# Optimization experiments

Measured on AMD Instinct MI355X. Metric: run time of the kernel, lower is better.

Reference implementation:

```python
import jax, jax.numpy as jnp
import numpy as np

D = 512        # latent_dim
DT = 256       # text_latent_dim
H = 8          # num_heads
TE = 2048      # time_embed_dim
NEG = -1000000.0


def _ln(x, g, b, eps=1e-5):
    m = jnp.mean(x, axis=-1, keepdims=True)
    v = jnp.mean(jnp.square(x - m), axis=-1, keepdims=True)
    return (x - m) * jax.lax.rsqrt(v + eps) * g + b


def _linear(x, W, b):
    return x @ W.T + b


def setup_inputs() -> dict:
    key = jax.random.key(0)
    ks = jax.random.split(key, 24)
    B, T, NT, R, LR = 32, 1024, 77, 4, 256
    inp = {
        'x': jax.random.normal(ks[0], (B, T, D), jnp.float32),
        'xf': jax.random.normal(ks[1], (B, NT, DT), jnp.float32),
        'emb': jax.random.normal(ks[2], (B, TE), jnp.float32),
        'src_mask': jax.random.randint(ks[3], (B, T, 1), 0, 2).astype(jnp.float32),
        'cond_type': jax.random.randint(ks[4], (B, 1, 1), 0, 100).astype(jnp.int32),
        're_motion': jax.random.normal(ks[5], (B, R, LR, D), jnp.float32),
        're_text': jax.random.normal(ks[6], (B, R, 1, D), jnp.float32),
        're_mask': jax.random.randint(ks[7], (B, R, LR), 0, 2).astype(jnp.float32),
    }
    s = 0.02
    def W(k, o, i):
        return jax.random.normal(k, (o, i), jnp.float32) * s
    params = {
        'norm_g': jnp.ones((D,), jnp.float32), 'norm_b': jnp.zeros((D,), jnp.float32),
        'tnorm_g': jnp.ones((DT,), jnp.float32), 'tnorm_b': jnp.zeros((DT,), jnp.float32),
        'rn1_g': jnp.ones((2 * D,), jnp.float32), 'rn1_b': jnp.zeros((2 * D,), jnp.float32),
        'rn2_g': jnp.ones((D,), jnp.float32), 'rn2_b': jnp.zeros((D,), jnp.float32),
        'Wq': W(ks[8], D, D), 'bq': jnp.zeros((D,), jnp.float32),
        'Wkt': W(ks[9], D, DT), 'bkt': jnp.zeros((D,), jnp.float32),
        'Wvt': W(ks[10], D, DT), 'bvt': jnp.zeros((D,), jnp.float32),
        'Wkm': W(ks[11], D, D), 'bkm': jnp.zeros((D,), jnp.float32),
        'Wvm': W(ks[12], D, D), 'bvm': jnp.zeros((D,), jnp.float32),
        'Wkr': W(ks[13], D, 2 * D), 'bkr': jnp.zeros((D,), jnp.float32),
        'Wvr': W(ks[14], D, D), 'bvr': jnp.zeros((D,), jnp.float32),
        'emb_W': W(ks[15], 2 * D, TE), 'emb_b': jnp.zeros((2 * D,), jnp.float32),
        'snorm_g': jnp.ones((D,), jnp.float32), 'snorm_b': jnp.zeros((D,), jnp.float32),
        'out_W': W(ks[16], D, D), 'out_b': jnp.zeros((D,), jnp.float32),
    }
    inp.update(params)
    return inp


def _forward(x, xf, emb, src_mask, cond_type, re_motion, re_text, re_mask,
             norm_g, norm_b, tnorm_g, tnorm_b, rn1_g, rn1_b, rn2_g, rn2_b,
             Wq, bq, Wkt, bkt, Wvt, bvt, Wkm, bkm, Wvm, bvm, Wkr, bkr, Wvr, bvr,
             emb_W, emb_b, snorm_g, snorm_b, out_W, out_b):
    B, T, _ = x.shape
    re_mask_r = re_mask.reshape(B, -1, 1)                       # [B, R*LR, 1]
    N = xf.shape[1] + T + re_motion.shape[1] * re_motion.shape[2]

    xn = _ln(x, norm_g, norm_b)                                  # [B,T,D]
    xfn = _ln(xf, tnorm_g, tnorm_b)                              # [B,NT,DT]
    query = _linear(xn, Wq, bq)                                  # [B,T,D]

    text_ct = (cond_type % 10 > 0).astype(x.dtype)               # [B,1,1]
    retr_ct = (cond_type // 10 > 0).astype(x.dtype)              # [B,1,1]

    re_text_rep = jnp.broadcast_to(re_text, re_motion.shape)     # repeat along Lr
    re_feat_key = jnp.concatenate([re_motion, re_text_rep], axis=-1).reshape(B, -1, 2 * D)

    k_text = _linear(xfn, Wkt, bkt) + (1.0 - text_ct) * NEG
    k_retr = (_linear(_ln(re_feat_key, rn1_g, rn1_b), Wkr, bkr)
              + (1.0 - retr_ct) * NEG + (1.0 - re_mask_r) * NEG)
    k_mot = _linear(xn, Wkm, bkm) + (1.0 - src_mask) * NEG
    key_cat = jnp.concatenate([k_text, k_retr, k_mot], axis=1)   # [B,N,D]

    q = jax.nn.softmax(query.reshape(B, T, H, -1), axis=-1)      # softmax over head_dim
    k = jax.nn.softmax(key_cat.reshape(B, N, H, -1), axis=1)     # softmax over tokens

    re_feat_value = re_motion.reshape(B, -1, D)
    v_text = _linear(xfn, Wvt, bvt) * text_ct
    v_retr = _linear(_ln(re_feat_value, rn2_g, rn2_b), Wvr, bvr) * retr_ct * re_mask_r
    v_mot = _linear(xn, Wvm, bvm) * src_mask
    v = jnp.concatenate([v_text, v_retr, v_mot], axis=1).reshape(B, N, H, -1)

    attention = jnp.einsum('bnhd,bnhl->bhdl', k, v)              # [B,H,hd,hd]
    y = jnp.einsum('bthd,bhdl->bthl', q, attention).reshape(B, T, D)

    # StylizationBlock: film-style scale/shift from time embedding, zero-init out proj
    emb_out = _linear(jax.nn.silu(emb), emb_W, emb_b)[:, None, :]  # [B,1,2D]
    scale, shift = emb_out[..., :D], emb_out[..., D:]
    h = _ln(y, snorm_g, snorm_b) * (1.0 + scale) + shift
    h = _linear(jax.nn.silu(h), out_W, out_b)
    return x + h


def reference(x, xf, emb, src_mask, cond_type, re_motion, re_text, re_mask,
              norm_g, norm_b, tnorm_g, tnorm_b, rn1_g, rn1_b, rn2_g, rn2_b,
              Wq, bq, Wkt, bkt, Wvt, bvt, Wkm, bkm, Wvm, bvm, Wkr, bkr, Wvr, bvr,
              emb_W, emb_b, snorm_g, snorm_b, out_W, out_b):
    return _forward(x, xf, emb, src_mask, cond_type, re_motion, re_text, re_mask,
                    norm_g, norm_b, tnorm_g, tnorm_b, rn1_g, rn1_b, rn2_g, rn2_b,
                    Wq, bq, Wkt, bkt, Wvt, bvt, Wkm, bkm, Wvm, bvm, Wkr, bkr, Wvr, bvr,
                    emb_W, emb_b, snorm_g, snorm_b, out_W, out_b)
```

## Files before the change

### kernel.cpp

```cpp
#include <hip/hip_runtime.h>
#include <cstddef>
#include <cstdint>

#define DEV __device__ __forceinline__

namespace {

constexpr int kH = 8;
constexpr int kB = 32, kT = 1024, kNT = 77, kR = 4, kLR = 256;
constexpr int kRL = kR * kLR;
constexpr float kNEG = -1000000.0f;
constexpr int kNtot = 2304;
constexpr int kNS2 = 3;
constexpr int kLDSW = 136;

typedef __bf16 bf16x8 __attribute__((ext_vector_type(8)));
typedef float f32x4 __attribute__((ext_vector_type(4)));

DEV unsigned short f2bf(float f) {
  unsigned int u = __float_as_uint(f);
  u += 0x7fffu + ((u >> 16) & 1u);
  return (unsigned short)(u >> 16);
}
DEV float bf2f(unsigned short h) { return __uint_as_float(((unsigned int)h) << 16); }

DEV float wave_sum(float v) {
  #pragma unroll
  for (int s = 32; s; s >>= 1) v += __shfl_xor(v, s);
  return v;
}

template<int COLS>
__global__ __launch_bounds__(256) void ln_bf16(const float* __restrict__ in,
    const float* __restrict__ g, const float* __restrict__ be,
    unsigned short* __restrict__ out) {
  constexpr int PT = COLS / 256;
  int row = blockIdx.x;
  const float* p = in + (size_t)row * COLS;
  unsigned short* o = out + (size_t)row * COLS;
  float v[PT]; float s = 0.f, s2 = 0.f;
  #pragma unroll
  for (int i = 0; i < PT; i++) {
    v[i] = p[threadIdx.x + i * 256];
    s += v[i]; s2 += v[i] * v[i];
  }
  __shared__ float red[2][4];
  int lane = threadIdx.x & 63, w = threadIdx.x >> 6;
  s = wave_sum(s); s2 = wave_sum(s2);
  if (!lane) { red[0][w] = s; red[1][w] = s2; }
  __syncthreads();
  s = red[0][0] + red[0][1] + red[0][2] + red[0][3];
  s2 = red[1][0] + red[1][1] + red[1][2] + red[1][3];
  float mean = s / COLS;
  float var = s2 / COLS - mean * mean;
  float rstd = rsqrtf(var + 1e-5f);
  #pragma unroll
  for (int i = 0; i < PT; i++) {
    int c = threadIdx.x + i * 256;
    o[c] = f2bf((v[i] - mean) * rstd * g[c] + be[c]);
  }
}

__global__ __launch_bounds__(256) void rfk_norm(const float* __restrict__ mot,
    const float* __restrict__ txt,
    const float* __restrict__ g1, const float* __restrict__ b1,
    const float* __restrict__ g2, const float* __restrict__ b2,
    unsigned short* __restrict__ rfk, unsigned short* __restrict__ rfv) {
  int m = blockIdx.x;
  const float* pm = mot + (size_t)m * 512;
  const float* pt = txt + (size_t)(m >> 8) * 512;
  float v[2], t[2];
  float sv = 0.f, sv2 = 0.f, st = 0.f, st2 = 0.f;
  #pragma unroll
  for (int i = 0; i < 2; i++) {
    v[i] = pm[threadIdx.x + i * 256]; sv += v[i]; sv2 += v[i] * v[i];
    t[i] = pt[threadIdx.x + i * 256]; st += t[i]; st2 += t[i] * t[i];
  }
  __shared__ float red[4][4];
  int lane = threadIdx.x & 63, w = threadIdx.x >> 6;
  sv = wave_sum(sv); sv2 = wave_sum(sv2); st = wave_sum(st); st2 = wave_sum(st2);
  if (!lane) { red[0][w] = sv; red[1][w] = sv2; red[2][w] = st; red[3][w] = st2; }
  __syncthreads();
  float SV = red[0][0] + red[0][1] + red[0][2] + red[0][3];
  float SV2 = red[1][0] + red[1][1] + red[1][2] + red[1][3];
  float ST = red[2][0] + red[2][1] + red[2][2] + red[2][3];
  float ST2 = red[3][0] + red[3][1] + red[3][2] + red[3][3];
  float SA = SV + ST, SA2 = SV2 + ST2;
  float ma = SA / 1024.f, va = SA2 / 1024.f - ma * ma;
  float ra_ = rsqrtf(va + 1e-5f);
  float mv = SV / 512.f, vv = SV2 / 512.f - mv * mv;
  float rv_ = rsqrtf(vv + 1e-5f);
  #pragma unroll
  for (int i = 0; i < 2; i++) {
    int c = threadIdx.x + i * 256;
    rfk[(size_t)m * 1024 + c]       = f2bf((v[i] - ma) * ra_ * g1[c] + b1[c]);
    rfk[(size_t)m * 1024 + 512 + c] = f2bf((t[i] - ma) * ra_ * g1[512 + c] + b1[512 + c]);
    rfv[(size_t)m * 512 + c]        = f2bf((v[i] - mv) * rv_ * g2[c] + b2[c]);
  }
}

__global__ __launch_bounds__(256) void rowmask_kernel(const int* __restrict__ ct,
    const float* __restrict__ src_mask, const float* __restrict__ re_mask,
    float* __restrict__ kaT, float* __restrict__ kaR, float* __restrict__ kaM,
    float* __restrict__ vmT, float* __restrict__ vmR, float* __restrict__ vmM,
    int nB) {
  int i = blockIdx.x * 256 + threadIdx.x;
  if (i < nB * kRL) {
    int b = i >> 10;
    int c = ct[b];
    float retr = (c / 10 > 0) ? 1.f : 0.f;
    float rm = re_mask[i];
    kaR[i] = (1.f - retr) * kNEG + (1.f - rm) * kNEG;
    vmR[i] = retr * rm;
    float sm = src_mask[i];
    kaM[i] = (1.f - sm) * kNEG;
    vmM[i] = sm;
  }
  if (i < nB * kNT) {
    int b = i / kNT;
    int c = ct[b];
    float text = (c % 10 > 0) ? 1.f : 0.f;
    kaT[i] = (1.f - text) * kNEG;
    vmT[i] = text;
  }
}

__global__ __launch_bounds__(256) void castw(const float* __restrict__ s,
    unsigned short* __restrict__ d, int n) {
  int i = (blockIdx.x * 256 + threadIdx.x) * 4;
  if (i < n) {
    float4 v = *reinterpret_cast<const float4*>(s + i);
    ushort4 o;
    o.x = f2bf(v.x); o.y = f2bf(v.y); o.z = f2bf(v.z); o.w = f2bf(v.w);
    *reinterpret_cast<ushort4*>(d + i) = o;
  }
}

__global__ __launch_bounds__(256) void zpad_kernel(unsigned short* __restrict__ E,
    unsigned short* __restrict__ V, int rows) {
  int i = blockIdx.x * 256 + threadIdx.x;
  if (i >= rows * 24) return;
  int row = i / 24, c = i % 24;
  size_t off = (size_t)row * kNtot + 2112 + c * 8;
  ulonglong2 z; z.x = 0; z.y = 0;
  *reinterpret_cast<ulonglong2*>(E + off) = z;
  *reinterpret_cast<ulonglong2*>(V + off) = z;
}

__global__ __launch_bounds__(256) void silu_emb(const float* __restrict__ emb,
    float* __restrict__ semb) {
  int i = (blockIdx.x * 256 + threadIdx.x) * 4;
  float4 v = *reinterpret_cast<const float4*>(emb + i);
  float4 o;
  o.x = v.x / (1.f + __expf(-v.x));
  o.y = v.y / (1.f + __expf(-v.y));
  o.z = v.z / (1.f + __expf(-v.z));
  o.w = v.w / (1.f + __expf(-v.w));
  *reinterpret_cast<float4*>(semb + i) = o;
}

__global__ __launch_bounds__(256) void emb_gemv2(const float* __restrict__ semb,
    const float* __restrict__ W, float* __restrict__ part) {
  int n = blockIdx.x * 4 + (threadIdx.x >> 6);
  int s = blockIdx.y;
  int lane = threadIdx.x & 63;
  int k = s * 256 + lane * 4;
  float4 wv = *reinterpret_cast<const float4*>(&W[(size_t)n * 2048 + k]);
  float acc[32];
  #pragma unroll
  for (int m = 0; m < 32; m++) {
    float4 sv = *reinterpret_cast<const float4*>(&semb[(size_t)m * 2048 + k]);
    acc[m] = fmaf(sv.x, wv.x, fmaf(sv.y, wv.y, fmaf(sv.z, wv.z, sv.w * wv.w)));
  }
  #pragma unroll
  for (int m = 0; m < 32; m++) {
    float t = wave_sum(acc[m]);
    if (lane == 0) part[((size_t)s * 32 + m) * 1024 + n] = t;
  }
}
__global__ __launch_bounds__(256) void emb_fin(const float* __restrict__ part,
    const float* __restrict__ bias, float* __restrict__ ss) {
  int i = blockIdx.x * 256 + threadIdx.x;
  float s = 0.f;
  #pragma unroll
  for (int c = 0; c < 8; c++) s += part[(size_t)c * 32768 + i];
  ss[i] = s + bias[i & 1023];
}

template<int OUTMODE, int TR>
__global__ __launch_bounds__(256) void gemm_mfma(
    const unsigned short* __restrict__ A, const unsigned short* __restrict__ W,
    const float* __restrict__ bias, void* __restrict__ Cout,
    int M, int K, int m_per_b, int n_total, int out_off,
    const float* __restrict__ rowAdd, const float* __restrict__ rowMul,
    const float* __restrict__ addX) {
  __shared__ __align__(16) char smem[34816];
  unsigned short* lds = (unsigned short*)smem;
  const int tid = threadIdx.x;
  const int lane = tid & 63;
  const int wv = tid >> 6;
  const int wr = (wv >> 1) * 64;
  const int wc = (wv & 1) * 64;
  const int m0 = blockIdx.y * 128;
  const int n0 = blockIdx.x * 128;

  const unsigned short* srcA[2]; const unsigned short* srcB[2];
  int dstOff[2];
  #pragma unroll
  for (int i = 0; i < 2; i++) {
    int lin = i * 256 + tid;
    int r = lin >> 2, cl = lin & 3;
    int cs = cl ^ ((r >> 1) & 3);
    int ra = m0 + r; if (ra > M - 1) ra = M - 1;
    srcA[i] = A + (size_t)ra * K + cs * 8;
    srcB[i] = W + (size_t)(n0 + r) * K + cs * 8;
    dstOff[i] = lin * 8;
  }
  int offA[4], offB[4];
  #pragma unroll
  for (int i = 0; i < 4; i++) {
    int r = wr + i * 16 + (lane & 15);
    int c = (lane >> 4) ^ ((r >> 1) & 3);
    offA[i] = r * 32 + c * 8;
    int rb = wc + i * 16 + (lane & 15);
    int cb = (lane >> 4) ^ ((rb >> 1) & 3);
    offB[i] = rb * 32 + cb * 8;
  }

  f32x4 acc[4][4] = {};

  #pragma unroll
  for (int i = 0; i < 2; i++) {
    __builtin_amdgcn_global_load_lds(
        (const __attribute__((address_space(1))) void*)(srcA[i]),
        (__attribute__((address_space(3))) void*)&lds[dstOff[i]], 16, 0, 0);
    __builtin_amdgcn_global_load_lds(
        (const __attribute__((address_space(1))) void*)(srcB[i]),
        (__attribute__((address_space(3))) void*)&lds[4096 + dstOff[i]], 16, 0, 0);
  }
  __syncthreads();

  int c = 0;
  for (int k0 = 0; k0 < K; k0 += 32) {
    int nc = c ^ 1;
    if (k0 + 32 < K) {
      #pragma unroll
      for (int i = 0; i < 2; i++) {
        __builtin_amdgcn_global_load_lds(
            (const __attribute__((address_space(1))) void*)(srcA[i] + k0 + 32),
            (__attribute__((address_space(3))) void*)&lds[nc * 8192 + dstOff[i]], 16, 0, 0);
        __builtin_amdgcn_global_load_lds(
            (const __attribute__((address_space(1))) void*)(srcB[i] + k0 + 32),
            (__attribute__((address_space(3))) void*)&lds[nc * 8192 + 4096 + dstOff[i]], 16, 0, 0);
      }
    }
    bf16x8 af[4], bf[4];
    #pragma unroll
    for (int i = 0; i < 4; i++) {
      af[i] = *reinterpret_cast<const bf16x8*>(&lds[c * 8192 + offA[i]]);
      bf[i] = *reinterpret_cast<const bf16x8*>(&lds[c * 8192 + 4096 + offB[i]]);
    }
    #pragma unroll
    for (int i = 0; i < 4; i++)
      #pragma unroll
      for (int j = 0; j < 4; j++)
        acc[i][j] = __builtin_amdgcn_mfma_f32_16x16x32_bf16(af[i], bf[j], acc[i][j], 0, 0, 0);
    __syncthreads();
    c = nc;
  }

  const int r4 = (lane >> 4) << 2;
  const int colb = n0 + wc + (lane & 15);
  const int rowb = m0 + wr + r4;

  if (OUTMODE != 0 && TR && (m_per_b & 7)) {
    unsigned short* C16 = (unsigned short*)Cout;
    #pragma unroll
    for (int i = 0; i < 4; i++) {
      #pragma unroll
      for (int r = 0; r < 4; r++) {
        int row = rowb + i * 16 + r;
        if (row >= M) continue;
        float ra = rowAdd ? rowAdd[row] : 0.f;
        float rm = rowMul ? rowMul[row] : 1.f;
        size_t nn = out_off + (row % m_per_b);
        size_t cb = (size_t)(row / m_per_b) * 512;
        #pragma unroll
        for (int j = 0; j < 4; j++) {
          int col = colb + j * 16;
          float v = (acc[i][j][r] + bias[col] + ra) * rm;
          if (OUTMODE == 2) v = __expf(v);
          C16[(cb + col) * kNtot + nn] = f2bf(v);
        }
      }
    }
    return;
  }

  if (OUTMODE != 0) {
    unsigned short* S = (unsigned short*)smem;
    #pragma unroll
    for (int i = 0; i < 4; i++) {
      #pragma unroll
      for (int r = 0; r < 4; r++) {
        int row_t = wr + i * 16 + r4 + r;
        int rowg = m0 + row_t; if (rowg > M - 1) rowg = M - 1;
        float ra = rowAdd ? rowAdd[rowg] : 0.f;
        float rm = rowMul ? rowMul[rowg] : 1.f;
        int key = TR ? (((row_t >> 3) & 7) << 3) : 0;
        #pragma unroll
        for (int j = 0; j < 4; j++) {
          int col_t = wc + j * 16 + (lane & 15);
          float v = (acc[i][j][r] + bias[n0 + col_t] + ra) * rm;
          if (OUTMODE == 2) v = __expf(v);
          S[row_t * kLDSW + (col_t ^ key)] = f2bf(v);
        }
      }
    }
    __syncthreads();
    if (TR) {
      #pragma unroll
      for (int it = 0; it < 8; it++) {
        int slot = it * 256 + tid;
        int col_t = slot >> 4;
        int mcx = slot & 15;
        int mc = mcx * 8;
        int key = (mcx & 7) << 3;
        union { unsigned short u[8]; ulonglong2 v; } w;
        #pragma unroll
        for (int e = 0; e < 8; e++)
          w.u[e] = S[(mc + e) * kLDSW + (col_t ^ key)];
        int row = m0 + mc;
        size_t obase = ((size_t)(row / m_per_b) * 512 + n0 + col_t) * (size_t)kNtot
                     + out_off + (row % m_per_b);
        *reinterpret_cast<ulonglong2*>((unsigned short*)Cout + obase) = w.v;
      }
    } else {
      #pragma unroll
      for (int it = 0; it < 8; it++) {
        int slot = it * 256 + tid;
        int row_t = slot >> 4;
        int cs = (slot & 15) * 8;
        int row = m0 + row_t;
        if (row < M) {
          size_t orow = (size_t)(row / m_per_b) * n_total + out_off + (row % m_per_b);
          ulonglong2 d = *reinterpret_cast<const ulonglong2*>(&S[row_t * kLDSW + cs]);
          *reinterpret_cast<ulonglong2*>((unsigned short*)Cout + orow * 512 + n0 + cs) = d;
        }
      }
    }
  } else {
    float* Sf = (float*)smem;
    #pragma unroll
    for (int p = 0; p < 2; p++) {
      __syncthreads();
      #pragma unroll
      for (int i2 = 0; i2 < 2; i2++) {
        int i = p * 2 + i2;
        #pragma unroll
        for (int r = 0; r < 4; r++) {
          int row_t = wr + i * 16 + r4 + r;
          int srow = (row_t & 31) + ((row_t >> 6) << 5);
          int rowg = m0 + row_t; if (rowg > M - 1) rowg = M - 1;
          float ra = rowAdd ? rowAdd[rowg] : 0.f;
          float rm = rowMul ? rowMul[rowg] : 1.f;
          #pragma unroll
          for (int j = 0; j < 4; j++) {
            int col_t = wc + j * 16 + (lane & 15);
            Sf[srow * kLDSW + col_t] = (acc[i][j][r] + bias[n0 + col_t] + ra) * rm;
          }
        }
      }
      __syncthreads();
      #pragma unroll
      for (int it = 0; it < 8; it++) {
        int slot = it * 256 + tid;
        int srow = slot >> 5;
        int c4 = (slot & 31) * 4;
        int row_t = (srow & 31) + p * 32 + ((srow >> 5) << 6);
        int row = m0 + row_t;
        if (row < M) {
          size_t orow = (size_t)(row / m_per_b) * n_total + out_off + (row % m_per_b);
          float4 v = *reinterpret_cast<const float4*>(&Sf[srow * kLDSW + c4]);
          if (addX) {
            float4 xv = *reinterpret_cast<const float4*>(&addX[(size_t)row * 512 + n0 + c4]);
            v.x += xv.x; v.y += xv.y; v.z += xv.z; v.w += xv.w;
          }
          *reinterpret_cast<float4*>((float*)Cout + orow * 512 + n0 + c4) = v;
        }
      }
    }
  }
}

__global__ __launch_bounds__(256) void attp_kernel(const unsigned short* __restrict__ E,
    const unsigned short* __restrict__ V, float* __restrict__ part,
    float* __restrict__ part_cs) {
  int bh = blockIdx.x;
  int s = blockIdx.y;
  const unsigned short* Ep = E + (size_t)bh * 64 * kNtot;
  const unsigned short* Vp = V + (size_t)bh * 64 * kNtot;
  __shared__ __align__(16) char smem[34816];
  unsigned short* Elds = (unsigned short*)smem;
  unsigned short* Vlds = (unsigned short*)(smem + 17408);
  int tid = threadIdx.x, lane = tid & 63, wv = tid >> 6;
  f32x4 acc[4] = {};
  float csum = 0.f;
  int cd = tid & 63, cq = tid >> 6;
  const int arow = (wv * 16 + (lane & 15)) * 136 + ((lane >> 4) << 3);
  const int brow0 = ((lane & 15)) * 136 + ((lane >> 4) << 3);

  for (int it = 0; it < 6; it++) {
    int n0 = s * 768 + it * 128;
    __syncthreads();
    #pragma unroll
    for (int r = 0; r < 4; r++) {
      int ch = r * 256 + tid;
      int d = ch >> 4, off = (ch & 15) * 8;
      *reinterpret_cast<ulonglong2*>(&Elds[d * 136 + off]) =
          *reinterpret_cast<const ulonglong2*>(Ep + (size_t)d * kNtot + n0 + off);
      *reinterpret_cast<ulonglong2*>(&Vlds[d * 136 + off]) =
          *reinterpret_cast<const ulonglong2*>(Vp + (size_t)d * kNtot + n0 + off);
    }
    __syncthreads();
    #pragma unroll
    for (int ks = 0; ks < 4; ks++) {
      bf16x8 af = *reinterpret_cast<const bf16x8*>(&Elds[arow + ks * 32]);
      #pragma unroll
      for (int j = 0; j < 4; j++) {
        bf16x8 bf = *reinterpret_cast<const bf16x8*>(&Vlds[brow0 + j * 16 * 136 + ks * 32]);
        acc[j] = __builtin_amdgcn_mfma_f32_16x16x32_bf16(af, bf, acc[j], 0, 0, 0);
      }
    }
    #pragma unroll
    for (int k8 = 0; k8 < 4; k8++) {
      bf16x8 ev = *reinterpret_cast<const bf16x8*>(&Elds[cd * 136 + cq * 32 + k8 * 8]);
      const unsigned short* pu = reinterpret_cast<const unsigned short*>(&ev);
      #pragma unroll
      for (int e = 0; e < 8; e++) csum += bf2f(pu[e]);
    }
  }
  float* op = part + ((size_t)bh * kNS2 + s) * 4096;
  int dbase = wv * 16 + ((lane >> 4) << 2);
  #pragma unroll
  for (int j = 0; j < 4; j++)
    #pragma unroll
    for (int r = 0; r < 4; r++)
      op[(dbase + r) * 64 + j * 16 + (lane & 15)] = acc[j][r];
  __syncthreads();
  float* csu = (float*)smem;
  csu[cq * 64 + cd] = csum;
  __syncthreads();
  if (tid < 64)
    part_cs[((size_t)bh * kNS2 + s) * 64 + tid] =
        csu[tid] + csu[64 + tid] + csu[128 + tid] + csu[192 + tid];
}

__global__ __launch_bounds__(256) void attc_kernel(const float* __restrict__ part,
    const float* __restrict__ part_cs, unsigned short* __restrict__ attT) {
  int bh = blockIdx.x;
  __shared__ float at[64][65];
  __shared__ float sinv[64];
  int tid = threadIdx.x;
  if (tid < 64) {
    float s = 0.f;
    #pragma unroll
    for (int c = 0; c < kNS2; c++) s += part_cs[((size_t)bh * kNS2 + c) * 64 + tid];
    sinv[tid] = 1.f / s;
  }
  for (int i = tid; i < 4096; i += 256) {
    float s = 0.f;
    #pragma unroll
    for (int c = 0; c < kNS2; c++) s += part[((size_t)bh * kNS2 + c) * 4096 + i];
    at[i >> 6][i & 63] = s;
  }
  __syncthreads();
  for (int j = tid; j < 4096; j += 256) {
    int l = j >> 6, d = j & 63;
    attT[(size_t)bh * 4096 + j] = f2bf(at[d][l] * sinv[d]);
  }
}

__global__ __launch_bounds__(256) void y_mfma(const unsigned short* __restrict__ q,
    const unsigned short* __restrict__ attT, unsigned short* __restrict__ y) {
  int bh = blockIdx.x; int b = bh >> 3, h = bh & 7;
  int t0 = blockIdx.y * 128;
  __shared__ unsigned short bt[64][72];
  __shared__ float rs[128];
  __shared__ unsigned short ob[128][72];
  int tid = threadIdx.x, lane = tid & 63, wv = tid >> 6;
  int wr = wv * 32;
  for (int i = tid; i < 512; i += 256) {
    int row = i >> 3, c8 = (i & 7) * 8;
    *reinterpret_cast<ulonglong2*>(&bt[row][c8]) =
        *reinterpret_cast<const ulonglong2*>(attT + (size_t)bh * 4096 + row * 64 + c8);
  }
  const unsigned short* qp = q + ((size_t)(b * 1024 + t0 + wr)) * 512 + h * 64;
  bf16x8 af[2][2];
  #pragma unroll
  for (int i = 0; i < 2; i++) {
    int row = i * 16 + (lane & 15);
    #pragma unroll
    for (int s = 0; s < 2; s++)
      af[i][s] = *reinterpret_cast<const bf16x8*>(qp + (size_t)row * 512 + s * 32 + (lane >> 4) * 8);
  }
  #pragma unroll
  for (int i = 0; i < 2; i++) {
    float r = 0.f;
    #pragma unroll
    for (int s = 0; s < 2; s++) {
      const unsigned short* pu = reinterpret_cast<const unsigned short*>(&af[i][s]);
      #pragma unroll
      for (int e = 0; e < 8; e++) r += bf2f(pu[e]);
    }
    r += __shfl_xor(r, 16); r += __shfl_xor(r, 32);
    if (lane < 16) rs[wr + i * 16 + lane] = r;
  }
  __syncthreads();
  f32x4 acc[2][4] = {};
  #pragma unroll
  for (int s = 0; s < 2; s++) {
    #pragma unroll
    for (int j = 0; j < 4; j++) {
      bf16x8 bf = *reinterpret_cast<const bf16x8*>(&bt[j * 16 + (lane & 15)][s * 32 + (lane >> 4) * 8]);
      #pragma unroll
      for (int i = 0; i < 2; i++)
        acc[i][j] = __builtin_amdgcn_mfma_f32_16x16x32_bf16(af[i][s], bf, acc[i][j], 0, 0, 0);
    }
  }
  int r4 = (lane >> 4) << 2;
  #pragma unroll
  for (int i = 0; i < 2; i++) {
    #pragma unroll
    for (int r = 0; r < 4; r++) {
      int row = wr + i * 16 + r4 + r;
      float rinv = 1.f / rs[row];
      #pragma unroll
      for (int j = 0; j < 4; j++)
        ob[row][j * 16 + (lane & 15)] = f2bf(acc[i][j][r] * rinv);
    }
  }
  __syncthreads();
  for (int i = tid; i < 1024; i += 256) {
    int row = i >> 3, c8 = (i & 7) * 8;
    *reinterpret_cast<ulonglong2*>(y + ((size_t)(b * 1024 + t0 + row)) * 512 + h * 64 + c8) =
        *reinterpret_cast<const ulonglong2*>(&ob[row][c8]);
  }
}

__global__ __launch_bounds__(256) void mod_kernel(const unsigned short* __restrict__ y,
    const float* __restrict__ ss, const float* __restrict__ g, const float* __restrict__ be,
    unsigned short* __restrict__ h) {
  int row = blockIdx.x; int b = row >> 10;
  const unsigned short* p = y + (size_t)row * 512;
  unsigned short* o = h + (size_t)row * 512;
  float v[2]; float s = 0.f, s2 = 0.f;
  #pragma unroll
  for (int i = 0; i < 2; i++) {
    v[i] = bf2f(p[threadIdx.x + i * 256]);
    s += v[i]; s2 += v[i] * v[i];
  }
  __shared__ float red[2][4];
  int lane = threadIdx.x & 63, w = threadIdx.x >> 6;
  s = wave_sum(s); s2 = wave_sum(s2);
  if (!lane) { red[0][w] = s; red[1][w] = s2; }
  __syncthreads();
  s = red[0][0] + red[0][1] + red[0][2] + red[0][3];
  s2 = red[1][0] + red[1][1] + red[1][2] + red[1][3];
  float mean = s / 512.f, var = s2 / 512.f - mean * mean;
  float rstd = rsqrtf(var + 1e-5f);
  #pragma unroll
  for (int i = 0; i < 2; i++) {
    int c = threadIdx.x + i * 256;
    float val = (v[i] - mean) * rstd * g[c] + be[c];
    val = val * (1.f + ss[b * 1024 + c]) + ss[b * 1024 + 512 + c];
    o[c] = f2bf(val / (1.f + __expf(-val)));
  }
}

}

extern "C" void kernel_launch(void* const* d_in, const int* in_sizes, int n_in,
                              void* d_out, int out_size, void* d_ws, size_t ws_size,
                              hipStream_t stream) {
  const float* x        = (const float*)d_in[0];
  const float* xf       = (const float*)d_in[1];
  const float* emb      = (const float*)d_in[2];
  const float* src_mask = (const float*)d_in[3];
  const int*   cond     = (const int*)d_in[4];
  const float* re_motion= (const float*)d_in[5];
  const float* re_text  = (const float*)d_in[6];
  const float* re_mask  = (const float*)d_in[7];
  const float* norm_g = (const float*)d_in[8],  * norm_b = (const float*)d_in[9];
  const float* tnorm_g= (const float*)d_in[10], * tnorm_b= (const float*)d_in[11];
  const float* rn1_g  = (const float*)d_in[12], * rn1_b  = (const float*)d_in[13];
  const float* rn2_g  = (const float*)d_in[14], * rn2_b  = (const float*)d_in[15];
  const float* Wq  = (const float*)d_in[16], * bq  = (const float*)d_in[17];
  const float* Wkt = (const float*)d_in[18], * bkt = (const float*)d_in[19];
  const float* Wvt = (const float*)d_in[20], * bvt = (const float*)d_in[21];
  const float* Wkm = (const float*)d_in[22], * bkm = (const float*)d_in[23];
  const float* Wvm = (const float*)d_in[24], * bvm = (const float*)d_in[25];
  const float* Wkr = (const float*)d_in[26], * bkr = (const float*)d_in[27];
  const float* Wvr = (const float*)d_in[28], * bvr = (const float*)d_in[29];
  const float* emb_W = (const float*)d_in[30], * emb_b = (const float*)d_in[31];
  const float* snorm_g = (const float*)d_in[32], * snorm_b = (const float*)d_in[33];
  const float* out_W = (const float*)d_in[34], * out_b = (const float*)d_in[35];
  float* out = (float*)d_out;

  char* base = (char*)d_ws;
  size_t off = 0;
  auto ab = [&](size_t nb) { char* p = base + off; off = (off + nb + 255) & ~(size_t)255; return p; };

  unsigned short* wq_bf  = (unsigned short*)ab(512 * 512 * 2);
  unsigned short* wkt_bf = (unsigned short*)ab(512 * 256 * 2);
  unsigned short* wvt_bf = (unsigned short*)ab(512 * 256 * 2);
  unsigned short* wkm_bf = (unsigned short*)ab(512 * 512 * 2);
  unsigned short* wvm_bf = (unsigned short*)ab(512 * 512 * 2);
  unsigned short* wkr_bf = (unsigned short*)ab(512 * 1024 * 2);
  unsigned short* wvr_bf = (unsigned short*)ab(512 * 512 * 2);
  unsigned short* wout_bf= (unsigned short*)ab(512 * 512 * 2);
  float* semb_f   = (float*)ab((size_t)kB * 2048 * 4);
  float* part_emb = (float*)ab((size_t)8 * kB * 1024 * 4);
  float* ssb_full = (float*)ab((size_t)kB * 1024 * 4);
  float* kaT_full = (float*)ab((size_t)kB * kNT * 4);
  float* vmT_full = (float*)ab((size_t)kB * kNT * 4);
  float* kaR_full = (float*)ab((size_t)kB * kRL * 4);
  float* kaM_full = (float*)ab((size_t)kB * kT * 4);
  float* vmR_full = (float*)ab((size_t)kB * kRL * 4);
  float* vmM_full = (float*)ab((size_t)kB * kT * 4);
  const size_t fixed_off = off;

  auto pad = [](size_t n) { return (n + 255) & ~(size_t)255; };
  auto chunk_bytes = [&](size_t CH) -> size_t {
    size_t s = 0;
    s += pad(CH * 1024 * 512 * 2);
    s += pad(CH * kNT * 256 * 2);
    s += pad(CH * 1024 * 1024 * 2);
    s += pad(CH * 1024 * 512 * 2);
    s += pad(CH * 1024 * 512 * 2);
    s += pad((size_t)CH * 512 * kNtot * 2);
    s += pad((size_t)CH * 512 * kNtot * 2);
    s += pad(CH * 8 * 4096 * 2);
    s += pad(CH * 8 * (size_t)kNS2 * 4096 * 4);
    s += pad(CH * 8 * (size_t)kNS2 * 64 * 4);
    return s;
  };
  int CH = 32;
  while (CH > 1 && fixed_off + chunk_bytes(CH) > ws_size) CH >>= 1;

  auto cl = [&](const float* s, unsigned short* d, int n) {
    castw<<<dim3((n / 4 + 255) / 256), 256, 0, stream>>>(s, d, n);
  };
  cl(Wq,  wq_bf,  512 * 512);
  cl(Wkt, wkt_bf, 512 * 256);
  cl(Wvt, wvt_bf, 512 * 256);
  cl(Wkm, wkm_bf, 512 * 512);
  cl(Wvm, wvm_bf, 512 * 512);
  cl(Wkr, wkr_bf, 512 * 1024);
  cl(Wvr, wvr_bf, 512 * 512);
  cl(out_W, wout_bf, 512 * 512);

  rowmask_kernel<<<dim3(kB * 4), 256, 0, stream>>>(cond, src_mask, re_mask,
      kaT_full, kaR_full, kaM_full, vmT_full, vmR_full, vmM_full, kB);
  silu_emb<<<dim3(kB * 2048 / 1024), 256, 0, stream>>>(emb, semb_f);
  emb_gemv2<<<dim3(256, 8), 256, 0, stream>>>(semb_f, emb_W, part_emb);
  emb_fin<<<dim3(128), 256, 0, stream>>>(part_emb, emb_b, ssb_full);

  for (int b0 = 0; b0 < kB; b0 += CH) {
    off = fixed_off;
    const int MRc = CH * 1024;
    const int MTc = CH * kNT;

    unsigned short* xn_bf  = (unsigned short*)ab((size_t)MRc * 512 * 2);
    unsigned short* xfn_bf = (unsigned short*)ab((size_t)MTc * 256 * 2);
    unsigned short* rfk_bf = (unsigned short*)ab((size_t)MRc * 1024 * 2);
    unsigned short* rfv_bf = (unsigned short*)ab((size_t)MRc * 512 * 2);
    unsigned short* qb_bf  = (unsigned short*)ab((size_t)MRc * 512 * 2);
    unsigned short* kc_bf  = (unsigned short*)ab((size_t)CH * 512 * kNtot * 2);
    unsigned short* vb_bf  = (unsigned short*)ab((size_t)CH * 512 * kNtot * 2);
    unsigned short* attT = (unsigned short*)ab((size_t)CH * 8 * 4096 * 2);
    float* attp = (float*)ab((size_t)CH * 8 * kNS2 * 4096 * 4);
    float* part_cs = (float*)ab((size_t)CH * 8 * kNS2 * 64 * 4);
    unsigned short* yb16 = rfk_bf;
    unsigned short* h_bf = xn_bf;

    const float* x_c   = x + (size_t)b0 * kT * 512;
    const float* xf_c  = xf + (size_t)b0 * kNT * 256;
    const float* rm_c  = re_motion + (size_t)b0 * kRL * 512;
    const float* rt_c  = re_text + (size_t)b0 * kR * 512;
    float* out_c = out + (size_t)b0 * kT * 512;

    ln_bf16<512><<<dim3(MRc), 256, 0, stream>>>(x_c, norm_g, norm_b, xn_bf);
    ln_bf16<256><<<dim3(MTc), 256, 0, stream>>>(xf_c, tnorm_g, tnorm_b, xfn_bf);
    rfk_norm<<<dim3(MRc), 256, 0, stream>>>(rm_c, rt_c, rn1_g, rn1_b, rn2_g, rn2_b,
                                            rfk_bf, rfv_bf);
    zpad_kernel<<<dim3(CH * 48), 256, 0, stream>>>(kc_bf, vb_bf, CH * 512);

    gemm_mfma<2, 0><<<dim3(4, CH * 8), 256, 0, stream>>>(xn_bf, wq_bf, bq, qb_bf,
        MRc, 512, MRc, 0, 0, nullptr, nullptr, nullptr);
    gemm_mfma<2, 1><<<dim3(4, (MTc + 127) / 128), 256, 0, stream>>>(xfn_bf, wkt_bf, bkt, kc_bf,
        MTc, 256, kNT, 0, 0, kaT_full + (size_t)b0 * kNT, nullptr, nullptr);
    gemm_mfma<2, 1><<<dim3(4, CH * 8), 256, 0, stream>>>(rfk_bf, wkr_bf, bkr, kc_bf,
        MRc, 1024, kRL, 0, kNT, kaR_full + (size_t)b0 * kRL, nullptr, nullptr);
    gemm_mfma<2, 1><<<dim3(4, CH * 8), 256, 0, stream>>>(xn_bf, wkm_bf, bkm, kc_bf,
        MRc, 512, kT, 0, kNT + kRL, kaM_full + (size_t)b0 * kT, nullptr, nullptr);
    gemm_mfma<1, 1><<<dim3(4, (MTc + 127) / 128), 256, 0, stream>>>(xfn_bf, wvt_bf, bvt, vb_bf,
        MTc, 256, kNT, 0, 0, nullptr, vmT_full + (size_t)b0 * kNT, nullptr);
    gemm_mfma<1, 1><<<dim3(4, CH * 8), 256, 0, stream>>>(rfv_bf, wvr_bf, bvr, vb_bf,
        MRc, 512, kRL, 0, kNT, nullptr, vmR_full + (size_t)b0 * kRL, nullptr);
    gemm_mfma<1, 1><<<dim3(4, CH * 8), 256, 0, stream>>>(xn_bf, wvm_bf, bvm, vb_bf,
        MRc, 512, kT, 0, kNT + kRL, nullptr, vmM_full + (size_t)b0 * kT, nullptr);

    attp_kernel<<<dim3(CH * 8, kNS2), 256, 0, stream>>>(kc_bf, vb_bf, attp, part_cs);
    attc_kernel<<<dim3(CH * 8), 256, 0, stream>>>(attp, part_cs, attT);
    y_mfma<<<dim3(CH * 8, 8), 256, 0, stream>>>(qb_bf, attT, yb16);

    mod_kernel<<<dim3(MRc), 256, 0, stream>>>(yb16, ssb_full + (size_t)b0 * 1024,
                                              snorm_g, snorm_b, h_bf);
    gemm_mfma<0, 0><<<dim3(4, CH * 8), 256, 0, stream>>>(h_bf, wout_bf, out_b, out_c,
        MRc, 512, MRc, 0, 0, nullptr, nullptr, x_c);
  }
}
```

Before: 624.3 us.

## Fold retrieval LayerNorms into weights and apply row stats in GEMM epilogue

After: 648.8 us. +3.9%, slower.

```diff
diff --git a/kernel.cpp b/kernel.cpp
--- a/kernel.cpp
+++ b/kernel.cpp
@@ -61,11 +61,10 @@
   }
 }
 
-__global__ __launch_bounds__(256) void rfk_norm(const float* __restrict__ mot,
-    const float* __restrict__ txt,
-    const float* __restrict__ g1, const float* __restrict__ b1,
-    const float* __restrict__ g2, const float* __restrict__ b2,
-    unsigned short* __restrict__ rfk, unsigned short* __restrict__ rfv) {
+__global__ __launch_bounds__(256) void rfk_stats(const float* __restrict__ mot,
+    const float* __restrict__ txt, unsigned short* __restrict__ mot_bf,
+    float* __restrict__ s1k, float* __restrict__ s2k,
+    float* __restrict__ s1v, float* __restrict__ s2v) {
   int m = blockIdx.x;
   const float* pm = mot + (size_t)m * 512;
   const float* pt = txt + (size_t)(m >> 8) * 512;
@@ -81,21 +80,83 @@
   sv = wave_sum(sv); sv2 = wave_sum(sv2); st = wave_sum(st); st2 = wave_sum(st2);
   if (!lane) { red[0][w] = sv; red[1][w] = sv2; red[2][w] = st; red[3][w] = st2; }
   __syncthreads();
-  float SV = red[0][0] + red[0][1] + red[0][2] + red[0][3];
-  float SV2 = red[1][0] + red[1][1] + red[1][2] + red[1][3];
-  float ST = red[2][0] + red[2][1] + red[2][2] + red[2][3];
-  float ST2 = red[3][0] + red[3][1] + red[3][2] + red[3][3];
-  float SA = SV + ST, SA2 = SV2 + ST2;
-  float ma = SA / 1024.f, va = SA2 / 1024.f - ma * ma;
-  float ra_ = rsqrtf(va + 1e-5f);
-  float mv = SV / 512.f, vv = SV2 / 512.f - mv * mv;
-  float rv_ = rsqrtf(vv + 1e-5f);
-  #pragma unroll
-  for (int i = 0; i < 2; i++) {
-    int c = threadIdx.x + i * 256;
-    rfk[(size_t)m * 1024 + c]       = f2bf((v[i] - ma) * ra_ * g1[c] + b1[c]);
-    rfk[(size_t)m * 1024 + 512 + c] = f2bf((t[i] - ma) * ra_ * g1[512 + c] + b1[512 + c]);
-    rfv[(size_t)m * 512 + c]        = f2bf((v[i] - mv) * rv_ * g2[c] + b2[c]);
+  #pragma unroll
+  for (int i = 0; i < 2; i++)
+    mot_bf[(size_t)m * 512 + threadIdx.x + i * 256] = f2bf(v[i]);
+  if (threadIdx.x == 0) {
+    float SV = red[0][0] + red[0][1] + red[0][2] + red[0][3];
+    float SV2 = red[1][0] + red[1][1] + red[1][2] + red[1][3];
+    float ST = red[2][0] + red[2][1] + red[2][2] + red[2][3];
+    float ST2 = red[3][0] + red[3][1] + red[3][2] + red[3][3];
+    float SA = SV + ST, SA2 = SV2 + ST2;
+    float ma = SA / 1024.f, va = SA2 / 1024.f - ma * ma;
+    float ra = rsqrtf(va + 1e-5f);
+    float mv = SV / 512.f, vv = SV2 / 512.f - mv * mv;
+    float rv = rsqrtf(vv + 1e-5f);
+    s1k[m] = ra; s2k[m] = -ra * ma;
+    s1v[m] = rv; s2v[m] = -rv * mv;
+  }
+}
+
+__global__ __launch_bounds__(256) void prep_w(
+    const float* __restrict__ Wkr, const float* __restrict__ g1,
+    const float* __restrict__ b1, const float* __restrict__ bkr,
+    const float* __restrict__ Wvr, const float* __restrict__ g2,
+    const float* __restrict__ b2, const float* __restrict__ bvr,
+    unsigned short* __restrict__ w1lo, unsigned short* __restrict__ w2,
+    float* __restrict__ G1, float* __restrict__ B1,
+    float* __restrict__ G2, float* __restrict__ B2) {
+  int n = blockIdx.x;
+  int tid = threadIdx.x;
+  float gs = 0.f, bs = 0.f;
+  #pragma unroll
+  for (int i = 0; i < 4; i++) {
+    int k = tid + i * 256;
+    float w = Wkr[(size_t)n * 1024 + k];
+    float gv = g1[k];
+    gs += gv * w; bs += b1[k] * w;
+    if (i < 2) w1lo[(size_t)n * 512 + k] = f2bf(gv * w);
+  }
+  float g2s = 0.f, b2s = 0.f;
+  #pragma unroll
+  for (int i = 0; i < 2; i++) {
+    int k = tid + i * 256;
+    float w = Wvr[(size_t)n * 512 + k];
+    g2s += g2[k] * w; b2s += b2[k] * w;
+    w2[(size_t)n * 512 + k] = f2bf(g2[k] * w);
+  }
+  __shared__ float red[4][4];
+  int lane = tid & 63, w_ = tid >> 6;
+  gs = wave_sum(gs); bs = wave_sum(bs); g2s = wave_sum(g2s); b2s = wave_sum(b2s);
+  if (!lane) { red[0][w_] = gs; red[1][w_] = bs; red[2][w_] = g2s; red[3][w_] = b2s; }
+  __syncthreads();
+  if (tid == 0) {
+    G1[n] = red[0][0] + red[0][1] + red[0][2] + red[0][3];
+    B1[n] = red[1][0] + red[1][1] + red[1][2] + red[1][3] + bkr[n];
+    G2[n] = red[2][0] + red[2][1] + red[2][2] + red[2][3];
+    B2[n] = red[3][0] + red[3][1] + red[3][2] + red[3][3] + bvr[n];
+  }
+}
+
+__global__ __launch_bounds__(256) void text_T(const float* __restrict__ re_text,
+    const float* __restrict__ g1, const float* __restrict__ Wkr,
+    float* __restrict__ T) {
+  int m = blockIdx.x;
+  __shared__ float tr[512];
+  int tid = threadIdx.x;
+  #pragma unroll
+  for (int i = 0; i < 2; i++) {
+    int k = tid + i * 256;
+    tr[k] = re_text[(size_t)m * 512 + k] * g1[512 + k];
+  }
+  __syncthreads();
+  #pragma unroll
+  for (int i = 0; i < 2; i++) {
+    int n = tid + i * 256;
+    const float* wp = Wkr + (size_t)n * 1024 + 512;
+    float acc = 0.f;
+    for (int k = 0; k < 512; k++) acc = fmaf(tr[k], wp[k], acc);
+    T[(size_t)m * 512 + n] = acc;
   }
 }
 
@@ -187,13 +248,15 @@
   ss[i] = s + bias[i & 1023];
 }
 
-template<int OUTMODE, int TR>
+template<int OUTMODE, int TR, int EPI>
 __global__ __launch_bounds__(256) void gemm_mfma(
     const unsigned short* __restrict__ A, const unsigned short* __restrict__ W,
     const float* __restrict__ bias, void* __restrict__ Cout,
     int M, int K, int m_per_b, int n_total, int out_off,
     const float* __restrict__ rowAdd, const float* __restrict__ rowMul,
-    const float* __restrict__ addX) {
+    const float* __restrict__ addX,
+    const float* __restrict__ s1, const float* __restrict__ s2,
+    const float* __restrict__ Gv, const float* __restrict__ Tt) {
   __shared__ __align__(16) char smem[34816];
   unsigned short* lds = (unsigned short*)smem;
   const int tid = threadIdx.x;
@@ -273,6 +336,22 @@
   const int colb = n0 + wc + (lane & 15);
   const int rowb = m0 + wr + r4;
 
+  auto epival = [&](float accv, int rowg, int col) -> float {
+    float v;
+    if (EPI == 1) {
+      v = (accv + Tt[(size_t)(rowg >> 8) * 512 + col]) * s1[rowg]
+          + s2[rowg] * Gv[col] + bias[col] + rowAdd[rowg];
+    } else if (EPI == 2) {
+      v = (accv * s1[rowg] + s2[rowg] * Gv[col] + bias[col]) * rowMul[rowg];
+    } else {
+      float ra = rowAdd ? rowAdd[rowg] : 0.f;
+      float rm = rowMul ? rowMul[rowg] : 1.f;
+      v = (accv + bias[col] + ra) * rm;
+    }
+    if (OUTMODE == 2) v = __expf(v);
+    return v;
+  };
+
   if (OUTMODE != 0 && TR && (m_per_b & 7)) {
     unsigned short* C16 = (unsigned short*)Cout;
     #pragma unroll
@@ -281,16 +360,12 @@
       for (int r = 0; r < 4; r++) {
         int row = rowb + i * 16 + r;
         if (row >= M) continue;
-        float ra = rowAdd ? rowAdd[row] : 0.f;
-        float rm = rowMul ? rowMul[row] : 1.f;
         size_t nn = out_off + (row % m_per_b);
         size_t cb = (size_t)(row / m_per_b) * 512;
         #pragma unroll
         for (int j = 0; j < 4; j++) {
           int col = colb + j * 16;
-          float v = (acc[i][j][r] + bias[col] + ra) * rm;
-          if (OUTMODE == 2) v = __expf(v);
-          C16[(cb + col) * kNtot + nn] = f2bf(v);
+          C16[(cb + col) * kNtot + nn] = f2bf(epival(acc[i][j][r], row, col));
         }
       }
     }
@@ -305,15 +380,11 @@
       for (int r = 0; r < 4; r++) {
         int row_t = wr + i * 16 + r4 + r;
         int rowg = m0 + row_t; if (rowg > M - 1) rowg = M - 1;
-        float ra = rowAdd ? rowAdd[rowg] : 0.f;
-        float rm = rowMul ? rowMul[rowg] : 1.f;
         int key = TR ? (((row_t >> 3) & 7) << 3) : 0;
         #pragma unroll
         for (int j = 0; j < 4; j++) {
           int col_t = wc + j * 16 + (lane & 15);
-          float v = (acc[i][j][r] + bias[n0 + col_t] + ra) * rm;
-          if (OUTMODE == 2) v = __expf(v);
-          S[row_t * kLDSW + (col_t ^ key)] = f2bf(v);
+          S[row_t * kLDSW + (col_t ^ key)] = f2bf(epival(acc[i][j][r], rowg, n0 + col_t));
         }
       }
     }
@@ -362,11 +433,11 @@
           int row_t = wr + i * 16 + r4 + r;
           int srow = (row_t & 31) + ((row_t >> 6) << 5);
           int rowg = m0 + row_t; if (rowg > M - 1) rowg = M - 1;
-          float ra = rowAdd ? rowAdd[rowg] : 0.f;
-          float rm = rowMul ? rowMul[rowg] : 1.f;
           #pragma unroll
           for (int j = 0; j < 4; j++) {
             int col_t = wc + j * 16 + (lane & 15);
+            float ra = rowAdd ? rowAdd[rowg] : 0.f;
+            float rm = rowMul ? rowMul[rowg] : 1.f;
             Sf[srow * kLDSW + col_t] = (acc[i][j][r] + bias[n0 + col_t] + ra) * rm;
           }
         }
@@ -616,9 +687,12 @@
   unsigned short* wvt_bf = (unsigned short*)ab(512 * 256 * 2);
   unsigned short* wkm_bf = (unsigned short*)ab(512 * 512 * 2);
   unsigned short* wvm_bf = (unsigned short*)ab(512 * 512 * 2);
-  unsigned short* wkr_bf = (unsigned short*)ab(512 * 1024 * 2);
-  unsigned short* wvr_bf = (unsigned short*)ab(512 * 512 * 2);
   unsigned short* wout_bf= (unsigned short*)ab(512 * 512 * 2);
+  unsigned short* w1lo_bf= (unsigned short*)ab(512 * 512 * 2);
+  unsigned short* w2_bf  = (unsigned short*)ab(512 * 512 * 2);
+  float* G1 = (float*)ab(512 * 4); float* B1 = (float*)ab(512 * 4);
+  float* G2 = (float*)ab(512 * 4); float* B2 = (float*)ab(512 * 4);
+  float* Tbuf = (float*)ab((size_t)kB * kR * 512 * 4);
   float* semb_f   = (float*)ab((size_t)kB * 2048 * 4);
   float* part_emb = (float*)ab((size_t)8 * kB * 1024 * 4);
   float* ssb_full = (float*)ab((size_t)kB * 1024 * 4);
@@ -635,8 +709,8 @@
     size_t s = 0;
     s += pad(CH * 1024 * 512 * 2);
     s += pad(CH * kNT * 256 * 2);
-    s += pad(CH * 1024 * 1024 * 2);
     s += pad(CH * 1024 * 512 * 2);
+    s += 4 * pad(CH * 1024 * 4);
     s += pad(CH * 1024 * 512 * 2);
     s += pad((size_t)CH * 512 * kNtot * 2);
     s += pad((size_t)CH * 512 * kNtot * 2);
@@ -656,9 +730,10 @@
   cl(Wvt, wvt_bf, 512 * 256);
   cl(Wkm, wkm_bf, 512 * 512);
   cl(Wvm, wvm_bf, 512 * 512);
-  cl(Wkr, wkr_bf, 512 * 1024);
-  cl(Wvr, wvr_bf, 512 * 512);
   cl(out_W, wout_bf, 512 * 512);
+  prep_w<<<dim3(512), 256, 0, stream>>>(Wkr, rn1_g, rn1_b, bkr, Wvr, rn2_g, rn2_b, bvr,
+                                        w1lo_bf, w2_bf, G1, B1, G2, B2);
+  text_T<<<dim3(kB * kR), 256, 0, stream>>>(re_text, rn1_g, Wkr, Tbuf);
 
   rowmask_kernel<<<dim3(kB * 4), 256, 0, stream>>>(cond, src_mask, re_mask,
       kaT_full, kaR_full, kaM_full, vmT_full, vmR_full, vmM_full, kB);
@@ -673,15 +748,18 @@
 
     unsigned short* xn_bf  = (unsigned short*)ab((size_t)MRc * 512 * 2);
     unsigned short* xfn_bf = (unsigned short*)ab((size_t)MTc * 256 * 2);
-    unsigned short* rfk_bf = (unsigned short*)ab((size_t)MRc * 1024 * 2);
-    unsigned short* rfv_bf = (unsigned short*)ab((size_t)MRc * 512 * 2);
+    unsigned short* mot_bf = (unsigned short*)ab((size_t)MRc * 512 * 2);
+    float* s1k = (float*)ab((size_t)CH * 1024 * 4);
+    float* s2k = (float*)ab((size_t)CH * 1024 * 4);
+    float* s1v = (float*)ab((size_t)CH * 1024 * 4);
+    float* s2v = (float*)ab((size_t)CH * 1024 * 4);
     unsigned short* qb_bf  = (unsigned short*)ab((size_t)MRc * 512 * 2);
     unsigned short* kc_bf  = (unsigned short*)ab((size_t)CH * 512 * kNtot * 2);
     unsigned short* vb_bf  = (unsigned short*)ab((size_t)CH * 512 * kNtot * 2);
     unsigned short* attT = (unsigned short*)ab((size_t)CH * 8 * 4096 * 2);
     float* attp = (float*)ab((size_t)CH * 8 * kNS2 * 4096 * 4);
     float* part_cs = (float*)ab((size_t)CH * 8 * kNS2 * 64 * 4);
-    unsigned short* yb16 = rfk_bf;
+    unsigned short* yb16 = mot_bf;
     unsigned short* h_bf = xn_bf;
 
     const float* x_c   = x + (size_t)b0 * kT * 512;
@@ -692,24 +770,29 @@
 
     ln_bf16<512><<<dim3(MRc), 256, 0, stream>>>(x_c, norm_g, norm_b, xn_bf);
     ln_bf16<256><<<dim3(MTc), 256, 0, stream>>>(xf_c, tnorm_g, tnorm_b, xfn_bf);
-    rfk_norm<<<dim3(MRc), 256, 0, stream>>>(rm_c, rt_c, rn1_g, rn1_b, rn2_g, rn2_b,
-                                            rfk_bf, rfv_bf);
+    rfk_stats<<<dim3(MRc), 256, 0, stream>>>(rm_c, rt_c, mot_bf, s1k, s2k, s1v, s2v);
     zpad_kernel<<<dim3(CH * 48), 256, 0, stream>>>(kc_bf, vb_bf, CH * 512);
 
-    gemm_mfma<2, 0><<<dim3(4, CH * 8), 256, 0, stream>>>(xn_bf, wq_bf, bq, qb_bf,
-        MRc, 512, MRc, 0, 0, nullptr, nullptr, nullptr);
-    gemm_mfma<2, 1><<<dim3(4, (MTc + 127) / 128), 256, 0, stream>>>(xfn_bf, wkt_bf, bkt, kc_bf,
-        MTc, 256, kNT, 0, 0, kaT_full + (size_t)b0 * kNT, nullptr, nullptr);
-    gemm_mfma<2, 1><<<dim3(4, CH * 8), 256, 0, stream>>>(rfk_bf, wkr_bf, bkr, kc_bf,
-        MRc, 1024, kRL, 0, kNT, kaR_full + (size_t)b0 * kRL, nullptr, nullptr);
-    gemm_mfma<2, 1><<<dim3(4, CH * 8), 256, 0, stream>>>(xn_bf, wkm_bf, bkm, kc_bf,
-        MRc, 512, kT, 0, kNT + kRL, kaM_full + (size_t)b0 * kT, nullptr, nullptr);
-    gemm_mfma<1, 1><<<dim3(4, (MTc + 127) / 128), 256, 0, stream>>>(xfn_bf, wvt_bf, bvt, vb_bf,
-        MTc, 256, kNT, 0, 0, nullptr, vmT_full + (size_t)b0 * kNT, nullptr);
-    gemm_mfma<1, 1><<<dim3(4, CH * 8), 256, 0, stream>>>(rfv_bf, wvr_bf, bvr, vb_bf,
-        MRc, 512, kRL, 0, kNT, nullptr, vmR_full + (size_t)b0 * kRL, nullptr);
-    gemm_mfma<1, 1><<<dim3(4, CH * 8), 256, 0, stream>>>(xn_bf, wvm_bf, bvm, vb_bf,
-        MRc, 512, kT, 0, kNT + kRL, nullptr, vmM_full + (size_t)b0 * kT, nullptr);
+    gemm_mfma<2, 0, 0><<<dim3(4, CH * 8), 256, 0, stream>>>(xn_bf, wq_bf, bq, qb_bf,
+        MRc, 512, MRc, 0, 0, nullptr, nullptr, nullptr, nullptr, nullptr, nullptr, nullptr);
+    gemm_mfma<2, 1, 0><<<dim3(4, (MTc + 127) / 128), 256, 0, stream>>>(xfn_bf, wkt_bf, bkt, kc_bf,
+        MTc, 256, kNT, 0, 0, kaT_full + (size_t)b0 * kNT, nullptr, nullptr,
+        nullptr, nullptr, nullptr, nullptr);
+    gemm_mfma<2, 1, 1><<<dim3(4, CH * 8), 256, 0, stream>>>(mot_bf, w1lo_bf, B1, kc_bf,
+        MRc, 512, kRL, 0, kNT, kaR_full + (size_t)b0 * kRL, nullptr, nullptr,
+        s1k, s2k, G1, Tbuf + (size_t)b0 * kR * 512);
+    gemm_mfma<2, 1, 0><<<dim3(4, CH * 8), 256, 0, stream>>>(xn_bf, wkm_bf, bkm, kc_bf,
+        MRc, 512, kT, 0, kNT + kRL, kaM_full + (size_t)b0 * kT, nullptr, nullptr,
+        nullptr, nullptr, nullptr, nullptr);
+    gemm_mfma<1, 1, 0><<<dim3(4, (MTc + 127) / 128), 256, 0, stream>>>(xfn_bf, wvt_bf, bvt, vb_bf,
+        MTc, 256, kNT, 0, 0, nullptr, vmT_full + (size_t)b0 * kNT, nullptr,
+        nullptr, nullptr, nullptr, nullptr);
+    gemm_mfma<1, 1, 2><<<dim3(4, CH * 8), 256, 0, stream>>>(mot_bf, w2_bf, B2, vb_bf,
+        MRc, 512, kRL, 0, kNT, nullptr, vmR_full + (size_t)b0 * kRL, nullptr,
+        s1v, s2v, G2, nullptr);
+    gemm_mfma<1, 1, 0><<<dim3(4, CH * 8), 256, 0, stream>>>(xn_bf, wvm_bf, bvm, vb_bf,
+        MRc, 512, kT, 0, kNT + kRL, nullptr, vmM_full + (size_t)b0 * kT, nullptr,
+        nullptr, nullptr, nullptr, nullptr);
 
     attp_kernel<<<dim3(CH * 8, kNS2), 256, 0, stream>>>(kc_bf, vb_bf, attp, part_cs);
     attc_kernel<<<dim3(CH * 8), 256, 0, stream>>>(attp, part_cs, attT);
@@ -717,7 +800,8 @@
 
     mod_kernel<<<dim3(MRc), 256, 0, stream>>>(yb16, ssb_full + (size_t)b0 * 1024,
                                               snorm_g, snorm_b, h_bf);
-    gemm_mfma<0, 0><<<dim3(4, CH * 8), 256, 0, stream>>>(h_bf, wout_bf, out_b, out_c,
-        MRc, 512, MRc, 0, 0, nullptr, nullptr, x_c);
-  }
-}
+    gemm_mfma<0, 0, 0><<<dim3(4, CH * 8), 256, 0, stream>>>(h_bf, wout_bf, out_b, out_c,
+        MRc, 512, MRc, 0, 0, nullptr, nullptr, x_c,
+        nullptr, nullptr, nullptr, nullptr);
+  }
+}
```
